# Kernel tuning notes

Hardware: AMD Instinct MI355X
Metric: run time of the kernel (lower is better)

Reference implementation:

```python
import jax, jax.numpy as jnp
import numpy as np

C = 19          # EEG channels
NP = C * C      # 361 channel pairs
D = 256         # UNIFIED_FEATURE_DIM
H = 8           # num_heads
HD = D // H     # head dim


def _build_mask():
    # rel[p, q] = True iff key-pair q shares a channel with query-pair p
    idx = np.arange(NP)
    ci, cj = idx // C, idx % C
    rel = ((ci[:, None] == ci[None, :]) | (ci[:, None] == cj[None, :]) |
           (cj[:, None] == ci[None, :]) | (cj[:, None] == cj[None, :]))
    return jnp.asarray(rel.reshape(C, C, NP))  # (channel_i, j, key_pair)

MASK = _build_mask()


def setup_inputs() -> dict:
    key = jax.random.key(0)
    ks = jax.random.split(key, 6)
    s = 0.05
    return {
        "x": jax.random.normal(ks[0], (32, NP, D), jnp.float32),
        # 19 stacked nn.MultiheadAttention modules: in_proj (3D, D) = [Wq; Wk; Wv]
        "w_in": jax.random.normal(ks[1], (C, 3 * D, D), jnp.float32) * s,
        "b_in": jnp.zeros((C, 3 * D), jnp.float32),
        "w_out": jax.random.normal(ks[2], (C, D, D), jnp.float32) * s,
        "b_out": jnp.zeros((C, D), jnp.float32),
        # fusion: nn.Linear(D, D)
        "w_fuse": jax.random.normal(ks[3], (D, D), jnp.float32) * s,
        "b_fuse": jnp.zeros((D,), jnp.float32),
    }


def reference(x, w_in, b_in, w_out, b_out, w_fuse, b_fuse):
    # x: (B, 361, D). Pair p=(i,j) at index i*19+j uses attention module i,
    # query = x[:, p], keys/values = pairs sharing channel i or j (mask).
    B = x.shape[0]
    wq, wk, wv = w_in[:, :D], w_in[:, D:2 * D], w_in[:, 2 * D:]
    bq, bk, bv = b_in[:, :D], b_in[:, D:2 * D], b_in[:, 2 * D:]

    # Per-channel K/V projections over all 361 pairs: (C, B, NP, D)
    K = jnp.einsum('bnd,ced->cbne', x, wk) + bk[:, None, None, :]
    V = jnp.einsum('bnd,ced->cbne', x, wv) + bv[:, None, None, :]
    # Queries grouped by first channel i: x reshaped to (B, C, C, D)
    xq = x.reshape(B, C, C, D)
    Q = jnp.einsum('bcjd,ced->cbje', xq, wq) + bq[:, None, None, :]  # (C,B,C,D)

    Qh = Q.reshape(C, B, C, H, HD)
    Kh = K.reshape(C, B, NP, H, HD)
    Vh = V.reshape(C, B, NP, H, HD)

    scale = 1.0 / jnp.sqrt(jnp.asarray(HD, x.dtype))
    scores = jnp.einsum('cbqhe,cbkhe->cbhqk', Qh, Kh) * scale  # (C,B,H,C,NP)
    scores = jnp.where(MASK[:, None, None, :, :], scores, -jnp.inf)
    attn = jax.nn.softmax(scores, axis=-1)

    out = jnp.einsum('cbhqk,cbkhe->cbqhe', attn, Vh).reshape(C, B, C, D)
    out = jnp.einsum('cbqd,ced->cbqe', out, w_out) + b_out[:, None, None, :]
    out = out.transpose(1, 0, 2, 3).reshape(B, NP, D)  # back to (B, 361, D)

    # fusion ('linear') + residual
    return out @ w_fuse.T + b_fuse + x
```

## Files before the change

### kernel.cpp

```cpp
#include <hip/hip_runtime.h>

#define CC 19
#define NPOS 361
#define NPAD 384
#define DIM 256
#define TKEY 32
#define NTILES 12

#define LDS_BYTES 67584

using bf16x8 = __attribute__((ext_vector_type(8))) short;
using f16x4  = __attribute__((ext_vector_type(4))) _Float16;
using floatx4 = __attribute__((ext_vector_type(4))) float;
using uintx2 = __attribute__((ext_vector_type(2))) unsigned int;

__device__ __forceinline__ unsigned short f2bf(float f) {
  unsigned u = __builtin_bit_cast(unsigned, f);
  u += 0x7fffu + ((u >> 16) & 1u);
  return (unsigned short)(u >> 16);
}

__device__ __forceinline__ f16x4 pack4h(float a, float b, float c2, float d) {
  const auto h01 = __builtin_amdgcn_cvt_pkrtz(a, b);
  const auto h23 = __builtin_amdgcn_cvt_pkrtz(c2, d);
  uintx2 uv = {__builtin_bit_cast(unsigned, h01), __builtin_bit_cast(unsigned, h23)};
  return __builtin_bit_cast(f16x4, uv);
}

__device__ __forceinline__ void gload_lds16(const void* g, void* l) {
  __builtin_amdgcn_global_load_lds(
      (const __attribute__((address_space(1))) void*)g,
      (__attribute__((address_space(3))) void*)l, 16, 0, 0);
}

__global__ void conv_all_kernel(const float* __restrict__ x,
                                const float* __restrict__ w_in,
                                const float* __restrict__ w_out,
                                const float* __restrict__ w_fuse,
                                unsigned short* __restrict__ ws) {
  const int j = blockIdx.x * 256 + threadIdx.x;
  float4 v = make_float4(0.f, 0.f, 0.f, 0.f);
  unsigned short* dst;
  if (j < 786432) {
    const int row = j >> 6;
    const int off = (j & 63) << 2;
    const int b = row / NPAD;
    const int r = row - b * NPAD;
    if (r < NPOS) v = *(const float4*)&x[(b * NPOS + r) * DIM + off];
    dst = &ws[row * DIM + off];
  } else if (j < 1720320) {
    const int k = j - 786432;
    v = *(const float4*)&w_in[k << 2];
    dst = &ws[3145728 + (k << 2)];
  } else if (j < 2031616) {
    const int k = j - 1720320;
    v = *(const float4*)&w_out[k << 2];
    dst = &ws[6881280 + (k << 2)];
  } else {
    const int k = j - 2031616;
    v = *(const float4*)&w_fuse[k << 2];
    dst = &ws[8126464 + (k << 2)];
  }
  ushort4 o;
  o.x = f2bf(v.x); o.y = f2bf(v.y); o.z = f2bf(v.z); o.w = f2bf(v.w);
  *(ushort4*)dst = o;
}

__launch_bounds__(256, 2)
__global__ void attn_kernel(const float* __restrict__ b_in,
                            const unsigned short* __restrict__ xbf,
                            const unsigned short* __restrict__ wibf,
                            float* __restrict__ out) {
  const int bid = blockIdx.x;
  const int xcd = bid & 7;
  const int slot = bid >> 3;
  const int c = slot >> 3;
  const int p = ((slot & 7) << 3) | xcd;
  const int b = p >> 1;
  const int hb = p & 1;

  const int tid = threadIdx.x;
  const int w = tid >> 6;
  const int lane = tid & 63;
  const int quad = lane >> 4;
  const int l16 = lane & 15;
  const int eh = (hb * 4 + w) * 32;

  extern __shared__ char smem[];
  char* sx = smem;
  unsigned* msk = (unsigned*)(smem + 65536);
  float* sL = (float*)(smem + 67072);

  const float scale = 0.25503486f;
  const floatx4 fzero = {0.f, 0.f, 0.f, 0.f};

  const int xw = (l16 & 7) << 4;
  const size_t xrowbytes = (size_t)b * NPAD * 512;

#pragma unroll
  for (int u = 0; u < 2; ++u) {
#pragma unroll
    for (int call = 0; call < 4; ++call) {
      const int sbyte = w * 4096 + call * 1024 + (lane << 4);
      const int row = sbyte >> 9;
      const int inner = (sbyte & 511) ^ ((row & 7) << 4);
      gload_lds16((const char*)xbf + xrowbytes + (size_t)(u * TKEY + row) * 512 + inner,
                  sx + u * 16384 + w * 4096 + call * 1024);
    }
  }

  f16x4 qf[2][2];
  {
    bf16x8 wq[2][8];
#pragma unroll
    for (int m4 = 0; m4 < 2; ++m4)
#pragma unroll
      for (int k = 0; k < 8; ++k)
        wq[m4][k] = *(const bf16x8*)&wibf[(c * 768 + eh + m4 * 16 + l16) * DIM + k * 32 + quad * 8];
    float bq[2][4];
#pragma unroll
    for (int m4 = 0; m4 < 2; ++m4) {
      const float4 bv4 = *(const float4*)&b_in[c * 768 + eh + m4 * 16 + quad * 4];
      bq[m4][0] = bv4.x; bq[m4][1] = bv4.y; bq[m4][2] = bv4.z; bq[m4][3] = bv4.w;
    }
#pragma unroll
    for (int mt = 0; mt < 2; ++mt) {
      const int xrow = b * NPAD + c * CC + mt * 16 + l16;
      bf16x8 xq[8];
#pragma unroll
      for (int k = 0; k < 8; ++k)
        xq[k] = *(const bf16x8*)&xbf[xrow * DIM + k * 32 + quad * 8];
#pragma unroll
      for (int m4 = 0; m4 < 2; ++m4) {
        floatx4 acc = fzero;
#pragma unroll
        for (int k = 0; k < 8; ++k)
          acc = __builtin_amdgcn_mfma_f32_16x16x32_bf16(wq[m4][k], xq[k], acc, 0, 0, 0);
        qf[mt][m4] = pack4h((acc[0] + bq[m4][0]) * scale, (acc[1] + bq[m4][1]) * scale,
                            (acc[2] + bq[m4][2]) * scale, (acc[3] + bq[m4][3]) * scale);
      }
    }
  }

  bf16x8 wk[2][8], wv[2][8];
#pragma unroll
  for (int m4 = 0; m4 < 2; ++m4)
#pragma unroll
    for (int k = 0; k < 8; ++k) {
      wk[m4][k] =
          *(const bf16x8*)&wibf[(c * 768 + 256 + eh + m4 * 16 + l16) * DIM + k * 32 + quad * 8];
      wv[m4][k] =
          *(const bf16x8*)&wibf[(c * 768 + 512 + eh + m4 * 16 + l16) * DIM + k * 32 + quad * 8];
    }
  float bV[2];
#pragma unroll
  for (int ne = 0; ne < 2; ++ne) bV[ne] = b_in[c * 768 + 512 + eh + ne * 16 + l16];

  for (int e2 = tid; e2 < 384; e2 += 256) {
    const int q = e2 / 12;
    const int wd = e2 - q * 12;
    unsigned m = 0u;
    for (int i = 0; i < 32; ++i) {
      const int kabs = wd * 32 + i;
      const unsigned ki = ((unsigned)kabs * 110377u) >> 21;
      const unsigned kj = (unsigned)kabs - ki * 19u;
      if (kabs < NPOS && (ki == (unsigned)c || kj == (unsigned)c ||
                          ki == (unsigned)q || kj == (unsigned)q))
        m |= (1u << i);
    }
    msk[e2] = m;
  }

  floatx4 o_acc[2][2];
  float lsum[2] = {0.f, 0.f};
#pragma unroll
  for (int mt = 0; mt < 2; ++mt)
#pragma unroll
    for (int ne = 0; ne < 2; ++ne) o_acc[mt][ne] = fzero;

  __syncthreads();

  for (int s6 = 0; s6 < 6; ++s6) {
    const int tb = s6 * 2;
    if (s6 < 5) {
#pragma unroll
      for (int u = 0; u < 2; ++u) {
        const int t = tb + 2 + u;
        char* bxn = sx + (t & 3) * 16384;
#pragma unroll
        for (int call = 0; call < 4; ++call) {
          const int sbyte = w * 4096 + call * 1024 + (lane << 4);
          const int row = sbyte >> 9;
          const int inner = (sbyte & 511) ^ ((row & 7) << 4);
          gload_lds16((const char*)xbf + xrowbytes + (size_t)(t * TKEY + row) * 512 + inner,
                      bxn + w * 4096 + call * 1024);
        }
      }
    }

#pragma unroll
    for (int u = 0; u < 2; ++u) {
      const int t = tb + u;
      const char* bx = sx + (t & 3) * 16384;

      floatx4 aK[2][2], aV[2][2];
#pragma unroll
      for (int i = 0; i < 2; ++i)
#pragma unroll
        for (int j = 0; j < 2; ++j) { aK[i][j] = fzero; aV[i][j] = fzero; }
      __builtin_amdgcn_s_setprio(1);
#pragma unroll
      for (int k = 0; k < 8; ++k) {
        bf16x8 xfr[2];
#pragma unroll
        for (int n4 = 0; n4 < 2; ++n4) {
          const int row = n4 * 16 + l16;
          const int inner = (k * 64 + quad * 16) ^ xw;
          xfr[n4] = *(const bf16x8*)(bx + row * 512 + inner);
        }
#pragma unroll
        for (int m4 = 0; m4 < 2; ++m4)
#pragma unroll
          for (int n4 = 0; n4 < 2; ++n4) {
            aK[m4][n4] = __builtin_amdgcn_mfma_f32_16x16x32_bf16(wk[m4][k], xfr[n4], aK[m4][n4], 0, 0, 0);
            aV[n4][m4] = __builtin_amdgcn_mfma_f32_16x16x32_bf16(xfr[n4], wv[m4][k], aV[n4][m4], 0, 0, 0);
          }
      }
      __builtin_amdgcn_s_setprio(0);

      f16x4 kf[2][2];
      f16x4 vf[2][2];
#pragma unroll
      for (int kt = 0; kt < 2; ++kt)
#pragma unroll
        for (int ec = 0; ec < 2; ++ec) {
          kf[kt][ec] = pack4h(aK[ec][kt][0], aK[ec][kt][1], aK[ec][kt][2], aK[ec][kt][3]);
          vf[kt][ec] = pack4h(aV[kt][ec][0], aV[kt][ec][1], aV[kt][ec][2], aV[kt][ec][3]);
        }

#pragma unroll
      for (int mt = 0; mt < 2; ++mt) {
        const int q = mt * 16 + l16;
        const unsigned mw = msk[q * 12 + t];
        f16x4 pf[2];
#pragma unroll
        for (int kt = 0; kt < 2; ++kt) {
          floatx4 s2 = __builtin_amdgcn_mfma_f32_16x16x16f16(kf[kt][0], qf[mt][0], fzero, 0, 0, 0);
          s2 = __builtin_amdgcn_mfma_f32_16x16x16f16(kf[kt][1], qf[mt][1], s2, 0, 0, 0);
          const unsigned mk = mw >> (kt * 16 + quad * 4);
          float p[4];
#pragma unroll
          for (int r = 0; r < 4; ++r)
            p[r] = (mk & (1u << r)) ? __builtin_exp2f(s2[r]) : 0.f;
          lsum[mt] += (p[0] + p[1]) + (p[2] + p[3]);
          pf[kt] = pack4h(p[0], p[1], p[2], p[3]);
        }
        __builtin_amdgcn_s_setprio(1);
#pragma unroll
        for (int kt = 0; kt < 2; ++kt)
#pragma unroll
          for (int ne = 0; ne < 2; ++ne)
            o_acc[mt][ne] =
                __builtin_amdgcn_mfma_f32_16x16x16f16(pf[kt], vf[kt][ne], o_acc[mt][ne], 0, 0, 0);
        __builtin_amdgcn_s_setprio(0);
      }
    }
    if (s6 < 5) __syncthreads();
  }

#pragma unroll
  for (int mt = 0; mt < 2; ++mt) {
    lsum[mt] += __shfl_xor(lsum[mt], 16);
    lsum[mt] += __shfl_xor(lsum[mt], 32);
  }
  if (lane < 16) {
    sL[w * 32 + lane] = lsum[0];
    sL[w * 32 + 16 + lane] = lsum[1];
  }
  float invl[2][4];
#pragma unroll
  for (int mt = 0; mt < 2; ++mt)
#pragma unroll
    for (int r = 0; r < 4; ++r)
      invl[mt][r] = 1.f / sL[w * 32 + mt * 16 + quad * 4 + r];

  unsigned short* aop = (unsigned short*)(out + (size_t)(b * NPOS + c * CC) * DIM);
#pragma unroll
  for (int mt = 0; mt < 2; ++mt)
#pragma unroll
    for (int ne = 0; ne < 2; ++ne)
#pragma unroll
      for (int r = 0; r < 4; ++r) {
        const int q = mt * 16 + quad * 4 + r;
        if (q < CC)
          aop[q * DIM + eh + ne * 16 + l16] =
              f2bf(o_acc[mt][ne][r] * invl[mt][r] + bV[ne]);
      }
}

__launch_bounds__(512)
__global__ void epi_kernel(const float* __restrict__ xf,
                           const float* __restrict__ b_out,
                           const float* __restrict__ b_fuse,
                           const unsigned short* __restrict__ wobf,
                           const unsigned short* __restrict__ wfbf,
                           float* __restrict__ out) {
  const int bid = blockIdx.x;
  const int xcd = bid & 7;
  const int slot = bid >> 3;
  const int c = slot >> 2;
  const int b = ((slot & 3) << 3) | xcd;

  const int tid = threadIdx.x;
  const int w = tid >> 6;
  const int lane = tid & 63;
  const int quad = lane >> 4;
  const int l16 = lane & 15;

  __shared__ unsigned short sA[32 * 264];
  __shared__ unsigned short sT[32 * 264];

  const size_t fbase = (size_t)(b * NPOS + c * CC) * DIM;
  const unsigned short* aop = (const unsigned short*)(out + fbase);
  const floatx4 fzero = {0.f, 0.f, 0.f, 0.f};
  const bf16x8 zero8 = {};

#pragma unroll
  for (int it = 0; it < 2; ++it) {
    const int cc2 = tid + it * 512;
    const int row = cc2 >> 5;
    const int col = (cc2 & 31) * 8;
    bf16x8 v = zero8;
    if (row < CC) v = *(const bf16x8*)&aop[row * DIM + col];
    *(bf16x8*)&sA[row * 264 + col] = v;
  }
  __syncthreads();

#pragma unroll
  for (int mt = 0; mt < 2; ++mt) {
    bf16x8 a8[8];
#pragma unroll
    for (int k = 0; k < 8; ++k)
      a8[k] = *(const bf16x8*)&sA[(mt * 16 + l16) * 264 + k * 32 + quad * 8];
#pragma unroll
    for (int nt2 = 0; nt2 < 2; ++nt2) {
      const int e0 = w * 32 + nt2 * 16;
      floatx4 acc = fzero;
#pragma unroll
      for (int k = 0; k < 8; ++k) {
        bf16x8 b8 = *(const bf16x8*)&wobf[(c * 256 + e0 + l16) * DIM + k * 32 + quad * 8];
        acc = __builtin_amdgcn_mfma_f32_16x16x32_bf16(a8[k], b8, acc, 0, 0, 0);
      }
      const float bias = b_out[c * 256 + e0 + l16];
#pragma unroll
      for (int r = 0; r < 4; ++r)
        sT[(mt * 16 + quad * 4 + r) * 264 + e0 + l16] = f2bf(acc[r] + bias);
    }
  }
  __syncthreads();

#pragma unroll
  for (int mt = 0; mt < 2; ++mt) {
    bf16x8 a8[8];
#pragma unroll
    for (int k = 0; k < 8; ++k)
      a8[k] = *(const bf16x8*)&sT[(mt * 16 + l16) * 264 + k * 32 + quad * 8];
#pragma unroll
    for (int nt2 = 0; nt2 < 2; ++nt2) {
      const int e0 = w * 32 + nt2 * 16;
      floatx4 acc = fzero;
#pragma unroll
      for (int k = 0; k < 8; ++k) {
        bf16x8 b8 = *(const bf16x8*)&wfbf[(e0 + l16) * DIM + k * 32 + quad * 8];
        acc = __builtin_amdgcn_mfma_f32_16x16x32_bf16(a8[k], b8, acc, 0, 0, 0);
      }
      const float bfu = b_fuse[e0 + l16];
#pragma unroll
      for (int r = 0; r < 4; ++r) {
        const int row = mt * 16 + quad * 4 + r;
        if (row < CC) {
          const size_t gp = fbase + (size_t)row * DIM + e0 + l16;
          out[gp] = acc[r] + bfu + xf[gp];
        }
      }
    }
  }
}

extern "C" void kernel_launch(void* const* d_in, const int* in_sizes, int n_in,
                              void* d_out, int out_size, void* d_ws, size_t ws_size,
                              hipStream_t stream) {
  const float* x      = (const float*)d_in[0];
  const float* w_in   = (const float*)d_in[1];
  const float* b_in   = (const float*)d_in[2];
  const float* w_out  = (const float*)d_in[3];
  const float* b_out  = (const float*)d_in[4];
  const float* w_fuse = (const float*)d_in[5];
  const float* b_fuse = (const float*)d_in[6];
  float* out = (float*)d_out;

  if (ws_size < (size_t)16384000) return;

  unsigned short* ws = (unsigned short*)d_ws;
  unsigned short* x_bf  = ws;
  unsigned short* wi_bf = ws + 3145728;
  unsigned short* wo_bf = ws + 6881280;
  unsigned short* wf_bf = ws + 8126464;

  conv_all_kernel<<<8000, 256, 0, stream>>>(x, w_in, w_out, w_fuse, ws);

  (void)hipFuncSetAttribute((const void*)attn_kernel,
                            hipFuncAttributeMaxDynamicSharedMemorySize, LDS_BYTES);
  attn_kernel<<<1216, 256, LDS_BYTES, stream>>>(b_in, x_bf, wi_bf, out);

  epi_kernel<<<608, 512, 0, stream>>>(x, b_out, b_fuse, wo_bf, wf_bf, out);
}
```

Measured before the change: 233.5 us.

## Fold out-projection into fusion weight and software-pipeline attention softmax

```diff
diff --git a/kernel.cpp b/kernel.cpp
--- a/kernel.cpp
+++ b/kernel.cpp
@@ -20,6 +20,10 @@
   return (unsigned short)(u >> 16);
 }
 
+__device__ __forceinline__ float bf2f(unsigned short h) {
+  return __builtin_bit_cast(float, ((unsigned)h) << 16);
+}
+
 __device__ __forceinline__ f16x4 pack4h(float a, float b, float c2, float d) {
   const auto h01 = __builtin_amdgcn_cvt_pkrtz(a, b);
   const auto h23 = __builtin_amdgcn_cvt_pkrtz(c2, d);
@@ -35,7 +39,6 @@
 
 __global__ void conv_all_kernel(const float* __restrict__ x,
                                 const float* __restrict__ w_in,
-                                const float* __restrict__ w_out,
                                 const float* __restrict__ w_fuse,
                                 unsigned short* __restrict__ ws) {
   const int j = blockIdx.x * 256 + threadIdx.x;
@@ -52,18 +55,56 @@
     const int k = j - 786432;
     v = *(const float4*)&w_in[k << 2];
     dst = &ws[3145728 + (k << 2)];
-  } else if (j < 2031616) {
+  } else {
     const int k = j - 1720320;
-    v = *(const float4*)&w_out[k << 2];
-    dst = &ws[6881280 + (k << 2)];
-  } else {
-    const int k = j - 2031616;
     v = *(const float4*)&w_fuse[k << 2];
     dst = &ws[8126464 + (k << 2)];
   }
   ushort4 o;
   o.x = f2bf(v.x); o.y = f2bf(v.y); o.z = f2bf(v.z); o.w = f2bf(v.w);
   *(ushort4*)dst = o;
+}
+
+__launch_bounds__(512)
+__global__ void wcomb_kernel(const float* __restrict__ wof,
+                             const unsigned short* __restrict__ wfbf,
+                             unsigned short* __restrict__ wcbf) {
+  const int c = blockIdx.x >> 2;
+  const int fslab = blockIdx.x & 3;
+  const int tid = threadIdx.x;
+  const int w = tid >> 6;
+  const int lane = tid & 63;
+  const int quad = lane >> 4;
+  const int l16 = lane & 15;
+
+  const int f_w = fslab * 64 + (w & 3) * 16;
+  const int d0_w = (w >> 2) * 128;
+  const floatx4 fzero = {0.f, 0.f, 0.f, 0.f};
+
+  floatx4 acc[8];
+#pragma unroll
+  for (int nt = 0; nt < 8; ++nt) acc[nt] = fzero;
+
+  for (int kt = 0; kt < 8; ++kt) {
+    const bf16x8 a8 = *(const bf16x8*)&wfbf[(f_w + l16) * 256 + kt * 32 + quad * 8];
+#pragma unroll
+    for (int nt = 0; nt < 8; ++nt) {
+      const int d = d0_w + nt * 16 + l16;
+      bf16x8 bn;
+#pragma unroll
+      for (int j = 0; j < 8; ++j) {
+        const float v = wof[c * 65536 + (kt * 32 + quad * 8 + j) * 256 + d];
+        bn[j] = (short)f2bf(v);
+      }
+      acc[nt] = __builtin_amdgcn_mfma_f32_16x16x32_bf16(a8, bn, acc[nt], 0, 0, 0);
+    }
+  }
+#pragma unroll
+  for (int nt = 0; nt < 8; ++nt)
+#pragma unroll
+    for (int r = 0; r < 4; ++r)
+      wcbf[(c * 256 + f_w + quad * 4 + r) * 256 + d0_w + nt * 16 + l16] =
+          f2bf(acc[nt][r]);
 }
 
 __launch_bounds__(256, 2)
@@ -178,6 +219,14 @@
 #pragma unroll
     for (int ne = 0; ne < 2; ++ne) o_acc[mt][ne] = fzero;
 
+  floatx4 sp[2][2];
+  f16x4 vfp[2][2];
+  unsigned mwp[2] = {0u, 0u};
+#pragma unroll
+  for (int i = 0; i < 2; ++i)
+#pragma unroll
+    for (int j = 0; j < 2; ++j) { sp[i][j] = fzero; vfp[i][j] = pack4h(0.f, 0.f, 0.f, 0.f); }
+
   __syncthreads();
 
   for (int s6 = 0; s6 < 6; ++s6) {
@@ -228,44 +277,69 @@
       }
       __builtin_amdgcn_s_setprio(0);
 
+#pragma unroll
+      for (int mt = 0; mt < 2; ++mt) {
+        f16x4 pf[2];
+#pragma unroll
+        for (int kt = 0; kt < 2; ++kt) {
+          const unsigned mk = mwp[mt] >> (kt * 16 + quad * 4);
+          float p[4];
+#pragma unroll
+          for (int r = 0; r < 4; ++r)
+            p[r] = (mk & (1u << r)) ? __builtin_exp2f(sp[mt][kt][r]) : 0.f;
+          lsum[mt] += (p[0] + p[1]) + (p[2] + p[3]);
+          pf[kt] = pack4h(p[0], p[1], p[2], p[3]);
+        }
+#pragma unroll
+        for (int kt = 0; kt < 2; ++kt)
+#pragma unroll
+          for (int ne = 0; ne < 2; ++ne)
+            o_acc[mt][ne] =
+                __builtin_amdgcn_mfma_f32_16x16x16f16(pf[kt], vfp[kt][ne], o_acc[mt][ne], 0, 0, 0);
+      }
+
       f16x4 kf[2][2];
-      f16x4 vf[2][2];
 #pragma unroll
       for (int kt = 0; kt < 2; ++kt)
 #pragma unroll
         for (int ec = 0; ec < 2; ++ec) {
           kf[kt][ec] = pack4h(aK[ec][kt][0], aK[ec][kt][1], aK[ec][kt][2], aK[ec][kt][3]);
-          vf[kt][ec] = pack4h(aV[kt][ec][0], aV[kt][ec][1], aV[kt][ec][2], aV[kt][ec][3]);
+          vfp[kt][ec] = pack4h(aV[kt][ec][0], aV[kt][ec][1], aV[kt][ec][2], aV[kt][ec][3]);
         }
 
 #pragma unroll
       for (int mt = 0; mt < 2; ++mt) {
         const int q = mt * 16 + l16;
-        const unsigned mw = msk[q * 12 + t];
-        f16x4 pf[2];
+        mwp[mt] = msk[q * 12 + t];
 #pragma unroll
         for (int kt = 0; kt < 2; ++kt) {
           floatx4 s2 = __builtin_amdgcn_mfma_f32_16x16x16f16(kf[kt][0], qf[mt][0], fzero, 0, 0, 0);
-          s2 = __builtin_amdgcn_mfma_f32_16x16x16f16(kf[kt][1], qf[mt][1], s2, 0, 0, 0);
-          const unsigned mk = mw >> (kt * 16 + quad * 4);
-          float p[4];
-#pragma unroll
-          for (int r = 0; r < 4; ++r)
-            p[r] = (mk & (1u << r)) ? __builtin_exp2f(s2[r]) : 0.f;
-          lsum[mt] += (p[0] + p[1]) + (p[2] + p[3]);
-          pf[kt] = pack4h(p[0], p[1], p[2], p[3]);
-        }
-        __builtin_amdgcn_s_setprio(1);
-#pragma unroll
-        for (int kt = 0; kt < 2; ++kt)
-#pragma unroll
-          for (int ne = 0; ne < 2; ++ne)
-            o_acc[mt][ne] =
-                __builtin_amdgcn_mfma_f32_16x16x16f16(pf[kt], vf[kt][ne], o_acc[mt][ne], 0, 0, 0);
-        __builtin_amdgcn_s_setprio(0);
+          sp[mt][kt] = __builtin_amdgcn_mfma_f32_16x16x16f16(kf[kt][1], qf[mt][1], s2, 0, 0, 0);
+        }
       }
     }
     if (s6 < 5) __syncthreads();
+  }
+
+#pragma unroll
+  for (int mt = 0; mt < 2; ++mt) {
+    f16x4 pf[2];
+#pragma unroll
+    for (int kt = 0; kt < 2; ++kt) {
+      const unsigned mk = mwp[mt] >> (kt * 16 + quad * 4);
+      float p[4];
+#pragma unroll
+      for (int r = 0; r < 4; ++r)
+        p[r] = (mk & (1u << r)) ? __builtin_exp2f(sp[mt][kt][r]) : 0.f;
+      lsum[mt] += (p[0] + p[1]) + (p[2] + p[3]);
+      pf[kt] = pack4h(p[0], p[1], p[2], p[3]);
+    }
+#pragma unroll
+    for (int kt = 0; kt < 2; ++kt)
+#pragma unroll
+      for (int ne = 0; ne < 2; ++ne)
+        o_acc[mt][ne] =
+            __builtin_amdgcn_mfma_f32_16x16x16f16(pf[kt], vfp[kt][ne], o_acc[mt][ne], 0, 0, 0);
   }
 
 #pragma unroll
@@ -302,8 +376,8 @@
 __global__ void epi_kernel(const float* __restrict__ xf,
                            const float* __restrict__ b_out,
                            const float* __restrict__ b_fuse,
-                           const unsigned short* __restrict__ wobf,
                            const unsigned short* __restrict__ wfbf,
+                           const unsigned short* __restrict__ wcbf,
                            float* __restrict__ out) {
   const int bid = blockIdx.x;
   const int xcd = bid & 7;
@@ -318,7 +392,6 @@
   const int l16 = lane & 15;
 
   __shared__ unsigned short sA[32 * 264];
-  __shared__ unsigned short sT[32 * 264];
 
   const size_t fbase = (size_t)(b * NPOS + c * CC) * DIM;
   const unsigned short* aop = (const unsigned short*)(out + fbase);
@@ -334,6 +407,20 @@
     if (row < CC) v = *(const bf16x8*)&aop[row * DIM + col];
     *(bf16x8*)&sA[row * 264 + col] = v;
   }
+
+  float bc[2];
+#pragma unroll
+  for (int nt2 = 0; nt2 < 2; ++nt2) {
+    const int f = w * 32 + nt2 * 16 + l16;
+    float s = b_fuse[f];
+    for (int kk = 0; kk < 32; ++kk) {
+      const bf16x8 w8 = *(const bf16x8*)&wfbf[f * 256 + kk * 8];
+#pragma unroll
+      for (int j = 0; j < 8; ++j)
+        s += bf2f((unsigned short)w8[j]) * b_out[c * 256 + kk * 8 + j];
+    }
+    bc[nt2] = s;
+  }
   __syncthreads();
 
 #pragma unroll
@@ -348,39 +435,15 @@
       floatx4 acc = fzero;
 #pragma unroll
       for (int k = 0; k < 8; ++k) {
-        bf16x8 b8 = *(const bf16x8*)&wobf[(c * 256 + e0 + l16) * DIM + k * 32 + quad * 8];
+        bf16x8 b8 = *(const bf16x8*)&wcbf[(c * 256 + e0 + l16) * DIM + k * 32 + quad * 8];
         acc = __builtin_amdgcn_mfma_f32_16x16x32_bf16(a8[k], b8, acc, 0, 0, 0);
       }
-      const float bias = b_out[c * 256 + e0 + l16];
-#pragma unroll
-      for (int r = 0; r < 4; ++r)
-        sT[(mt * 16 + quad * 4 + r) * 264 + e0 + l16] = f2bf(acc[r] + bias);
-    }
-  }
-  __syncthreads();
-
-#pragma unroll
-  for (int mt = 0; mt < 2; ++mt) {
-    bf16x8 a8[8];
-#pragma unroll
-    for (int k = 0; k < 8; ++k)
-      a8[k] = *(const bf16x8*)&sT[(mt * 16 + l16) * 264 + k * 32 + quad * 8];
-#pragma unroll
-    for (int nt2 = 0; nt2 < 2; ++nt2) {
-      const int e0 = w * 32 + nt2 * 16;
-      floatx4 acc = fzero;
-#pragma unroll
-      for (int k = 0; k < 8; ++k) {
-        bf16x8 b8 = *(const bf16x8*)&wfbf[(e0 + l16) * DIM + k * 32 + quad * 8];
-        acc = __builtin_amdgcn_mfma_f32_16x16x32_bf16(a8[k], b8, acc, 0, 0, 0);
-      }
-      const float bfu = b_fuse[e0 + l16];
 #pragma unroll
       for (int r = 0; r < 4; ++r) {
         const int row = mt * 16 + quad * 4 + r;
         if (row < CC) {
           const size_t gp = fbase + (size_t)row * DIM + e0 + l16;
-          out[gp] = acc[r] + bfu + xf[gp];
+          out[gp] = acc[r] + bc[nt2] + xf[gp];
         }
       }
     }
@@ -404,14 +467,16 @@
   unsigned short* ws = (unsigned short*)d_ws;
   unsigned short* x_bf  = ws;
   unsigned short* wi_bf = ws + 3145728;
-  unsigned short* wo_bf = ws + 6881280;
+  unsigned short* wc_bf = ws + 6881280;
   unsigned short* wf_bf = ws + 8126464;
 
-  conv_all_kernel<<<8000, 256, 0, stream>>>(x, w_in, w_out, w_fuse, ws);
+  conv_all_kernel<<<6784, 256, 0, stream>>>(x, w_in, w_fuse, ws);
+
+  wcomb_kernel<<<76, 512, 0, stream>>>(w_out, wf_bf, wc_bf);
 
   (void)hipFuncSetAttribute((const void*)attn_kernel,
                             hipFuncAttributeMaxDynamicSharedMemorySize, LDS_BYTES);
   attn_kernel<<<1216, 256, LDS_BYTES, stream>>>(b_in, x_bf, wi_bf, out);
 
-  epi_kernel<<<608, 512, 0, stream>>>(x, b_out, b_fuse, wo_bf, wf_bf, out);
-}
+  epi_kernel<<<608, 512, 0, stream>>>(x, b_out, b_fuse, wf_bf, wc_bf, out);
+}
```

Measured after the change: 378.5 us. 1.62x slower.

## Stream K/V weights from global per k-step and halve LDS buffering for occupancy

Applied to the files above, without the earlier changes.

```diff
diff --git a/kernel.cpp b/kernel.cpp
--- a/kernel.cpp
+++ b/kernel.cpp
@@ -7,7 +7,7 @@
 #define TKEY 32
 #define NTILES 12
 
-#define LDS_BYTES 67584
+#define LDS_BYTES 34816
 
 using bf16x8 = __attribute__((ext_vector_type(8))) short;
 using f16x4  = __attribute__((ext_vector_type(4))) _Float16;
@@ -66,7 +66,7 @@
   *(ushort4*)dst = o;
 }
 
-__launch_bounds__(256, 2)
+__launch_bounds__(256, 3)
 __global__ void attn_kernel(const float* __restrict__ b_in,
                             const unsigned short* __restrict__ xbf,
                             const unsigned short* __restrict__ wibf,
@@ -88,8 +88,8 @@
 
   extern __shared__ char smem[];
   char* sx = smem;
-  unsigned* msk = (unsigned*)(smem + 65536);
-  float* sL = (float*)(smem + 67072);
+  unsigned* msk = (unsigned*)(smem + 32768);
+  float* sL = (float*)(smem + 34304);
 
   const float scale = 0.25503486f;
   const floatx4 fzero = {0.f, 0.f, 0.f, 0.f};
@@ -98,15 +98,12 @@
   const size_t xrowbytes = (size_t)b * NPAD * 512;
 
 #pragma unroll
-  for (int u = 0; u < 2; ++u) {
-#pragma unroll
-    for (int call = 0; call < 4; ++call) {
-      const int sbyte = w * 4096 + call * 1024 + (lane << 4);
-      const int row = sbyte >> 9;
-      const int inner = (sbyte & 511) ^ ((row & 7) << 4);
-      gload_lds16((const char*)xbf + xrowbytes + (size_t)(u * TKEY + row) * 512 + inner,
-                  sx + u * 16384 + w * 4096 + call * 1024);
-    }
+  for (int call = 0; call < 4; ++call) {
+    const int sbyte = w * 4096 + call * 1024 + (lane << 4);
+    const int row = sbyte >> 9;
+    const int inner = (sbyte & 511) ^ ((row & 7) << 4);
+    gload_lds16((const char*)xbf + xrowbytes + (size_t)row * 512 + inner,
+                sx + w * 4096 + call * 1024);
   }
 
   f16x4 qf[2][2];
@@ -142,16 +139,10 @@
     }
   }
 
-  bf16x8 wk[2][8], wv[2][8];
-#pragma unroll
-  for (int m4 = 0; m4 < 2; ++m4)
-#pragma unroll
-    for (int k = 0; k < 8; ++k) {
-      wk[m4][k] =
-          *(const bf16x8*)&wibf[(c * 768 + 256 + eh + m4 * 16 + l16) * DIM + k * 32 + quad * 8];
-      wv[m4][k] =
-          *(const bf16x8*)&wibf[(c * 768 + 512 + eh + m4 * 16 + l16) * DIM + k * 32 + quad * 8];
-    }
+  const unsigned short* wk0 = &wibf[(c * 768 + 256 + eh + l16) * DIM + quad * 8];
+  const unsigned short* wk1 = wk0 + 16 * DIM;
+  const unsigned short* wv0 = &wibf[(c * 768 + 512 + eh + l16) * DIM + quad * 8];
+  const unsigned short* wv1 = wv0 + 16 * DIM;
   float bV[2];
 #pragma unroll
   for (int ne = 0; ne < 2; ++ne) bV[ne] = b_in[c * 768 + 512 + eh + ne * 16 + l16];
@@ -180,92 +171,87 @@
 
   __syncthreads();
 
-  for (int s6 = 0; s6 < 6; ++s6) {
-    const int tb = s6 * 2;
-    if (s6 < 5) {
-#pragma unroll
-      for (int u = 0; u < 2; ++u) {
-        const int t = tb + 2 + u;
-        char* bxn = sx + (t & 3) * 16384;
-#pragma unroll
-        for (int call = 0; call < 4; ++call) {
-          const int sbyte = w * 4096 + call * 1024 + (lane << 4);
-          const int row = sbyte >> 9;
-          const int inner = (sbyte & 511) ^ ((row & 7) << 4);
-          gload_lds16((const char*)xbf + xrowbytes + (size_t)(t * TKEY + row) * 512 + inner,
-                      bxn + w * 4096 + call * 1024);
+  for (int t = 0; t < NTILES; ++t) {
+    if (t + 1 < NTILES) {
+      char* bxn = sx + ((t + 1) & 1) * 16384;
+#pragma unroll
+      for (int call = 0; call < 4; ++call) {
+        const int sbyte = w * 4096 + call * 1024 + (lane << 4);
+        const int row = sbyte >> 9;
+        const int inner = (sbyte & 511) ^ ((row & 7) << 4);
+        gload_lds16((const char*)xbf + xrowbytes + (size_t)((t + 1) * TKEY + row) * 512 + inner,
+                    bxn + w * 4096 + call * 1024);
+      }
+    }
+    const char* bx = sx + (t & 1) * 16384;
+
+    floatx4 aK[2][2], aV[2][2];
+#pragma unroll
+    for (int i = 0; i < 2; ++i)
+#pragma unroll
+      for (int j = 0; j < 2; ++j) { aK[i][j] = fzero; aV[i][j] = fzero; }
+    __builtin_amdgcn_s_setprio(1);
+#pragma unroll
+    for (int k = 0; k < 8; ++k) {
+      bf16x8 wkf[2], wvf[2];
+      wkf[0] = *(const bf16x8*)&wk0[k * 32];
+      wkf[1] = *(const bf16x8*)&wk1[k * 32];
+      wvf[0] = *(const bf16x8*)&wv0[k * 32];
+      wvf[1] = *(const bf16x8*)&wv1[k * 32];
+      bf16x8 xfr[2];
+#pragma unroll
+      for (int n4 = 0; n4 < 2; ++n4) {
+        const int row = n4 * 16 + l16;
+        const int inner = (k * 64 + quad * 16) ^ xw;
+        xfr[n4] = *(const bf16x8*)(bx + row * 512 + inner);
+      }
+#pragma unroll
+      for (int m4 = 0; m4 < 2; ++m4)
+#pragma unroll
+        for (int n4 = 0; n4 < 2; ++n4) {
+          aK[m4][n4] = __builtin_amdgcn_mfma_f32_16x16x32_bf16(wkf[m4], xfr[n4], aK[m4][n4], 0, 0, 0);
+          aV[n4][m4] = __builtin_amdgcn_mfma_f32_16x16x32_bf16(xfr[n4], wvf[m4], aV[n4][m4], 0, 0, 0);
         }
-      }
-    }
-
-#pragma unroll
-    for (int u = 0; u < 2; ++u) {
-      const int t = tb + u;
-      const char* bx = sx + (t & 3) * 16384;
-
-      floatx4 aK[2][2], aV[2][2];
-#pragma unroll
-      for (int i = 0; i < 2; ++i)
-#pragma unroll
-        for (int j = 0; j < 2; ++j) { aK[i][j] = fzero; aV[i][j] = fzero; }
+    }
+    __builtin_amdgcn_s_setprio(0);
+
+    f16x4 kf[2][2];
+    f16x4 vf[2][2];
+#pragma unroll
+    for (int kt = 0; kt < 2; ++kt)
+#pragma unroll
+      for (int ec = 0; ec < 2; ++ec) {
+        kf[kt][ec] = pack4h(aK[ec][kt][0], aK[ec][kt][1], aK[ec][kt][2], aK[ec][kt][3]);
+        vf[kt][ec] = pack4h(aV[kt][ec][0], aV[kt][ec][1], aV[kt][ec][2], aV[kt][ec][3]);
+      }
+
+#pragma unroll
+    for (int mt = 0; mt < 2; ++mt) {
+      const int q = mt * 16 + l16;
+      const unsigned mw = msk[q * 12 + t];
+      f16x4 pf[2];
+#pragma unroll
+      for (int kt = 0; kt < 2; ++kt) {
+        floatx4 s2 = __builtin_amdgcn_mfma_f32_16x16x16f16(kf[kt][0], qf[mt][0], fzero, 0, 0, 0);
+        s2 = __builtin_amdgcn_mfma_f32_16x16x16f16(kf[kt][1], qf[mt][1], s2, 0, 0, 0);
+        const unsigned mk = mw >> (kt * 16 + quad * 4);
+        float p2[4];
+#pragma unroll
+        for (int r = 0; r < 4; ++r)
+          p2[r] = (mk & (1u << r)) ? __builtin_exp2f(s2[r]) : 0.f;
+        lsum[mt] += (p2[0] + p2[1]) + (p2[2] + p2[3]);
+        pf[kt] = pack4h(p2[0], p2[1], p2[2], p2[3]);
+      }
       __builtin_amdgcn_s_setprio(1);
 #pragma unroll
-      for (int k = 0; k < 8; ++k) {
-        bf16x8 xfr[2];
-#pragma unroll
-        for (int n4 = 0; n4 < 2; ++n4) {
-          const int row = n4 * 16 + l16;
-          const int inner = (k * 64 + quad * 16) ^ xw;
-          xfr[n4] = *(const bf16x8*)(bx + row * 512 + inner);
-        }
-#pragma unroll
-        for (int m4 = 0; m4 < 2; ++m4)
-#pragma unroll
-          for (int n4 = 0; n4 < 2; ++n4) {
-            aK[m4][n4] = __builtin_amdgcn_mfma_f32_16x16x32_bf16(wk[m4][k], xfr[n4], aK[m4][n4], 0, 0, 0);
-            aV[n4][m4] = __builtin_amdgcn_mfma_f32_16x16x32_bf16(xfr[n4], wv[m4][k], aV[n4][m4], 0, 0, 0);
-          }
-      }
+      for (int kt = 0; kt < 2; ++kt)
+#pragma unroll
+        for (int ne = 0; ne < 2; ++ne)
+          o_acc[mt][ne] =
+              __builtin_amdgcn_mfma_f32_16x16x16f16(pf[kt], vf[kt][ne], o_acc[mt][ne], 0, 0, 0);
       __builtin_amdgcn_s_setprio(0);
-
-      f16x4 kf[2][2];
-      f16x4 vf[2][2];
-#pragma unroll
-      for (int kt = 0; kt < 2; ++kt)
-#pragma unroll
-        for (int ec = 0; ec < 2; ++ec) {
-          kf[kt][ec] = pack4h(aK[ec][kt][0], aK[ec][kt][1], aK[ec][kt][2], aK[ec][kt][3]);
-          vf[kt][ec] = pack4h(aV[kt][ec][0], aV[kt][ec][1], aV[kt][ec][2], aV[kt][ec][3]);
-        }
-
-#pragma unroll
-      for (int mt = 0; mt < 2; ++mt) {
-        const int q = mt * 16 + l16;
-        const unsigned mw = msk[q * 12 + t];
-        f16x4 pf[2];
-#pragma unroll
-        for (int kt = 0; kt < 2; ++kt) {
-          floatx4 s2 = __builtin_amdgcn_mfma_f32_16x16x16f16(kf[kt][0], qf[mt][0], fzero, 0, 0, 0);
-          s2 = __builtin_amdgcn_mfma_f32_16x16x16f16(kf[kt][1], qf[mt][1], s2, 0, 0, 0);
-          const unsigned mk = mw >> (kt * 16 + quad * 4);
-          float p[4];
-#pragma unroll
-          for (int r = 0; r < 4; ++r)
-            p[r] = (mk & (1u << r)) ? __builtin_exp2f(s2[r]) : 0.f;
-          lsum[mt] += (p[0] + p[1]) + (p[2] + p[3]);
-          pf[kt] = pack4h(p[0], p[1], p[2], p[3]);
-        }
-        __builtin_amdgcn_s_setprio(1);
-#pragma unroll
-        for (int kt = 0; kt < 2; ++kt)
-#pragma unroll
-          for (int ne = 0; ne < 2; ++ne)
-            o_acc[mt][ne] =
-                __builtin_amdgcn_mfma_f32_16x16x16f16(pf[kt], vf[kt][ne], o_acc[mt][ne], 0, 0, 0);
-        __builtin_amdgcn_s_setprio(0);
-      }
-    }
-    if (s6 < 5) __syncthreads();
+    }
+    if (t + 1 < NTILES) __syncthreads();
   }
 
 #pragma unroll
```

Measured after the change: 390.7 us. 67.3% more time.

## Fuse epilogue projections into attention kernel with 512-thread blocks

Applied to the files above, without the earlier changes.

```diff
diff --git a/kernel.cpp b/kernel.cpp
--- a/kernel.cpp
+++ b/kernel.cpp
@@ -7,7 +7,7 @@
 #define TKEY 32
 #define NTILES 12
 
-#define LDS_BYTES 67584
+#define LDS_BYTES 68096
 
 using bf16x8 = __attribute__((ext_vector_type(8))) short;
 using f16x4  = __attribute__((ext_vector_type(4))) _Float16;
@@ -66,25 +66,28 @@
   *(ushort4*)dst = o;
 }
 
-__launch_bounds__(256, 2)
-__global__ void attn_kernel(const float* __restrict__ b_in,
+__launch_bounds__(512, 2)
+__global__ void attn_kernel(const float* __restrict__ xf,
+                            const float* __restrict__ b_in,
+                            const float* __restrict__ b_out,
+                            const float* __restrict__ b_fuse,
                             const unsigned short* __restrict__ xbf,
                             const unsigned short* __restrict__ wibf,
+                            const unsigned short* __restrict__ wobf,
+                            const unsigned short* __restrict__ wfbf,
                             float* __restrict__ out) {
   const int bid = blockIdx.x;
   const int xcd = bid & 7;
   const int slot = bid >> 3;
-  const int c = slot >> 3;
-  const int p = ((slot & 7) << 3) | xcd;
-  const int b = p >> 1;
-  const int hb = p & 1;
+  const int c = slot >> 2;
+  const int b = ((slot & 3) << 3) | xcd;
 
   const int tid = threadIdx.x;
   const int w = tid >> 6;
   const int lane = tid & 63;
   const int quad = lane >> 4;
   const int l16 = lane & 15;
-  const int eh = (hb * 4 + w) * 32;
+  const int eh = w * 32;
 
   extern __shared__ char smem[];
   char* sx = smem;
@@ -100,12 +103,12 @@
 #pragma unroll
   for (int u = 0; u < 2; ++u) {
 #pragma unroll
-    for (int call = 0; call < 4; ++call) {
-      const int sbyte = w * 4096 + call * 1024 + (lane << 4);
+    for (int call = 0; call < 2; ++call) {
+      const int sbyte = w * 2048 + call * 1024 + (lane << 4);
       const int row = sbyte >> 9;
       const int inner = (sbyte & 511) ^ ((row & 7) << 4);
       gload_lds16((const char*)xbf + xrowbytes + (size_t)(u * TKEY + row) * 512 + inner,
-                  sx + u * 16384 + w * 4096 + call * 1024);
+                  sx + u * 16384 + w * 2048 + call * 1024);
     }
   }
 
@@ -156,9 +159,9 @@
 #pragma unroll
   for (int ne = 0; ne < 2; ++ne) bV[ne] = b_in[c * 768 + 512 + eh + ne * 16 + l16];
 
-  for (int e2 = tid; e2 < 384; e2 += 256) {
-    const int q = e2 / 12;
-    const int wd = e2 - q * 12;
+  if (tid < 384) {
+    const int q = tid / 12;
+    const int wd = tid - q * 12;
     unsigned m = 0u;
     for (int i = 0; i < 32; ++i) {
       const int kabs = wd * 32 + i;
@@ -168,7 +171,7 @@
                           ki == (unsigned)q || kj == (unsigned)q))
         m |= (1u << i);
     }
-    msk[e2] = m;
+    msk[tid] = m;
   }
 
   floatx4 o_acc[2][2];
@@ -188,12 +191,12 @@
         const int t = tb + 2 + u;
         char* bxn = sx + (t & 3) * 16384;
 #pragma unroll
-        for (int call = 0; call < 4; ++call) {
-          const int sbyte = w * 4096 + call * 1024 + (lane << 4);
+        for (int call = 0; call < 2; ++call) {
+          const int sbyte = w * 2048 + call * 1024 + (lane << 4);
           const int row = sbyte >> 9;
           const int inner = (sbyte & 511) ^ ((row & 7) << 4);
           gload_lds16((const char*)xbf + xrowbytes + (size_t)(t * TKEY + row) * 512 + inner,
-                      bxn + w * 4096 + call * 1024);
+                      bxn + w * 2048 + call * 1024);
         }
       }
     }
@@ -248,12 +251,12 @@
           floatx4 s2 = __builtin_amdgcn_mfma_f32_16x16x16f16(kf[kt][0], qf[mt][0], fzero, 0, 0, 0);
           s2 = __builtin_amdgcn_mfma_f32_16x16x16f16(kf[kt][1], qf[mt][1], s2, 0, 0, 0);
           const unsigned mk = mw >> (kt * 16 + quad * 4);
-          float p[4];
+          float p2[4];
 #pragma unroll
           for (int r = 0; r < 4; ++r)
-            p[r] = (mk & (1u << r)) ? __builtin_exp2f(s2[r]) : 0.f;
-          lsum[mt] += (p[0] + p[1]) + (p[2] + p[3]);
-          pf[kt] = pack4h(p[0], p[1], p[2], p[3]);
+            p2[r] = (mk & (1u << r)) ? __builtin_exp2f(s2[r]) : 0.f;
+          lsum[mt] += (p2[0] + p2[1]) + (p2[2] + p2[3]);
+          pf[kt] = pack4h(p2[0], p2[1], p2[2], p2[3]);
         }
         __builtin_amdgcn_s_setprio(1);
 #pragma unroll
@@ -284,57 +287,19 @@
     for (int r = 0; r < 4; ++r)
       invl[mt][r] = 1.f / sL[w * 32 + mt * 16 + quad * 4 + r];
 
-  unsigned short* aop = (unsigned short*)(out + (size_t)(b * NPOS + c * CC) * DIM);
+  unsigned short* sA = (unsigned short*)smem;
+  unsigned short* sT = (unsigned short*)(smem + 16896);
 #pragma unroll
   for (int mt = 0; mt < 2; ++mt)
 #pragma unroll
     for (int ne = 0; ne < 2; ++ne)
 #pragma unroll
-      for (int r = 0; r < 4; ++r) {
-        const int q = mt * 16 + quad * 4 + r;
-        if (q < CC)
-          aop[q * DIM + eh + ne * 16 + l16] =
-              f2bf(o_acc[mt][ne][r] * invl[mt][r] + bV[ne]);
-      }
-}
-
-__launch_bounds__(512)
-__global__ void epi_kernel(const float* __restrict__ xf,
-                           const float* __restrict__ b_out,
-                           const float* __restrict__ b_fuse,
-                           const unsigned short* __restrict__ wobf,
-                           const unsigned short* __restrict__ wfbf,
-                           float* __restrict__ out) {
-  const int bid = blockIdx.x;
-  const int xcd = bid & 7;
-  const int slot = bid >> 3;
-  const int c = slot >> 2;
-  const int b = ((slot & 3) << 3) | xcd;
-
-  const int tid = threadIdx.x;
-  const int w = tid >> 6;
-  const int lane = tid & 63;
-  const int quad = lane >> 4;
-  const int l16 = lane & 15;
-
-  __shared__ unsigned short sA[32 * 264];
-  __shared__ unsigned short sT[32 * 264];
+      for (int r = 0; r < 4; ++r)
+        sA[(mt * 16 + quad * 4 + r) * 264 + eh + ne * 16 + l16] =
+            f2bf(o_acc[mt][ne][r] * invl[mt][r] + bV[ne]);
+  __syncthreads();
 
   const size_t fbase = (size_t)(b * NPOS + c * CC) * DIM;
-  const unsigned short* aop = (const unsigned short*)(out + fbase);
-  const floatx4 fzero = {0.f, 0.f, 0.f, 0.f};
-  const bf16x8 zero8 = {};
-
-#pragma unroll
-  for (int it = 0; it < 2; ++it) {
-    const int cc2 = tid + it * 512;
-    const int row = cc2 >> 5;
-    const int col = (cc2 & 31) * 8;
-    bf16x8 v = zero8;
-    if (row < CC) v = *(const bf16x8*)&aop[row * DIM + col];
-    *(bf16x8*)&sA[row * 264 + col] = v;
-  }
-  __syncthreads();
 
 #pragma unroll
   for (int mt = 0; mt < 2; ++mt) {
@@ -411,7 +376,6 @@
 
   (void)hipFuncSetAttribute((const void*)attn_kernel,
                             hipFuncAttributeMaxDynamicSharedMemorySize, LDS_BYTES);
-  attn_kernel<<<1216, 256, LDS_BYTES, stream>>>(b_in, x_bf, wi_bf, out);
-
-  epi_kernel<<<608, 512, 0, stream>>>(x, b_out, b_fuse, wo_bf, wf_bf, out);
-}
+  attn_kernel<<<608, 512, LDS_BYTES, stream>>>(x, b_in, b_out, b_fuse, x_bf, wi_bf,
+                                               wo_bf, wf_bf, out);
+}
```

Result: no change. 237.0 us (+1.5%).
